# Optimization experiments

Measured on AMD Instinct MI355X. Metric: run time of the kernel, lower is better.

The kernel has to match this reference:

```python
import jax, jax.numpy as jnp
import numpy as np

B, N, F = 8, 500000, 1000000


def setup_inputs() -> dict:
    key = jax.random.key(0)
    k1, k2 = jax.random.split(key)
    vert = jax.random.normal(k1, (B, N, 3), dtype=jnp.float32)
    faces = jax.random.randint(k2, (F, 3), 0, N, dtype=jnp.int64)
    return {"vert": vert, "faces": faces}


def _uniform_laplacian(vert, faces):
    # vert: [B, N, 3], faces: [F, 3]
    n = vert.shape[1]
    i, j, k = faces[:, 0], faces[:, 1], faces[:, 2]
    # 6 directed edges per face: dst accumulates its neighbors' positions (src)
    dst = jnp.concatenate([i, i, j, j, k, k])  # [6F]
    src = jnp.concatenate([j, k, i, k, i, j])  # [6F]
    deg = jax.ops.segment_sum(jnp.ones_like(dst, dtype=vert.dtype), dst, num_segments=n)  # [N]
    nbr_sum = jax.vmap(lambda v: jax.ops.segment_sum(v[src], dst, num_segments=n))(vert)  # [B,N,3]
    # lap = mean(neighbors) - v  (uniform Laplacian: D^{-1} A - I)
    return nbr_sum / jnp.maximum(deg, 1.0)[None, :, None] - vert


def reference(vert, faces):
    lap = _uniform_laplacian(vert, faces)          # [B, N, 3]
    curve = jnp.sqrt(jnp.sum(lap * lap, axis=-1))  # [B, N] (L2 norm over xyz)
    return curve
```

## Files before the change

kernel.cpp:

```cpp
#include <hip/hip_runtime.h>
#include <hip/hip_fp16.h>
#include <math.h>

#define BATCH 8
#define NBUK_MAX 512
#define BSHIFT 10
#define CAPB 6656
#define PACK_MASK 0x7FFFFull
#define SCAN_T 256
#define SCAN_E 8
#define SCAN_TILE (SCAN_T * SCAN_E)

union H2U { __half2 h; unsigned u; };

__device__ __forceinline__ long long pack3(int v, int a, int b) {
    return (long long)(((unsigned long long)(unsigned)v) |
                       ((unsigned long long)(unsigned)a << 19) |
                       ((unsigned long long)(unsigned)b << 38));
}

__global__ __launch_bounds__(1024) void expand_repack_kernel(
        const int* __restrict__ faces,
        int* __restrict__ cursor,
        long long* __restrict__ recbuf,
        const float* __restrict__ vert,
        uint2* __restrict__ vh,
        int N, int F, int expBlocks) {
    if ((int)blockIdx.x < expBlocks) {
        __shared__ int hist[NBUK_MAX];
        __shared__ int sbuf[NBUK_MAX];
        __shared__ int lbase[NBUK_MAX];
        __shared__ int gb[NBUK_MAX];
        __shared__ long long stage[3072];
        int tid = threadIdx.x;
        for (int x = tid; x < NBUK_MAX; x += 1024) hist[x] = 0;
        __syncthreads();

        int f = blockIdx.x * 1024 + tid;
        bool valid = f < F;
        int bb0 = 0, bb1 = 0, bb2 = 0, rr0 = 0, rr1 = 0, rr2 = 0;
        long long rc0 = 0, rc1 = 0, rc2 = 0;
        if (valid) {
            int i = faces[3 * f + 0];
            int j = faces[3 * f + 1];
            int k = faces[3 * f + 2];
            rc0 = pack3(i, j, k);
            rc1 = pack3(j, i, k);
            rc2 = pack3(k, i, j);
            bb0 = i >> BSHIFT; bb1 = j >> BSHIFT; bb2 = k >> BSHIFT;
            rr0 = atomicAdd(&hist[bb0], 1);
            rr1 = atomicAdd(&hist[bb1], 1);
            rr2 = atomicAdd(&hist[bb2], 1);
        }
        __syncthreads();

        if (tid < NBUK_MAX) sbuf[tid] = hist[tid];
        __syncthreads();
        for (int d = 1; d < NBUK_MAX; d <<= 1) {
            int t = 0;
            if (tid < NBUK_MAX && tid >= d) t = sbuf[tid - d];
            __syncthreads();
            if (tid < NBUK_MAX) sbuf[tid] += t;
            __syncthreads();
        }
        if (tid < NBUK_MAX) {
            lbase[tid] = sbuf[tid] - hist[tid];
            gb[tid] = (hist[tid] > 0) ? atomicAdd(&cursor[tid * 16], hist[tid]) : 0;
        }
        __syncthreads();

        if (valid) {
            stage[lbase[bb0] + rr0] = rc0;
            stage[lbase[bb1] + rr1] = rc1;
            stage[lbase[bb2] + rr2] = rc2;
        }
        __syncthreads();

        int total = sbuf[NBUK_MAX - 1];
        for (int t = tid; t < total; t += 1024) {
            long long r = stage[t];
            int v = (int)((unsigned long long)r & PACK_MASK);
            int b = v >> BSHIFT;
            int gpos = gb[b] + (t - lbase[b]);
            if (gpos < CAPB)
                recbuf[(size_t)b * CAPB + gpos] = r;
        }
    } else {
        int u = (blockIdx.x - expBlocks) * 1024 + threadIdx.x;
        if (u < N * BATCH) {
            int v = u >> 3;
            int b = u & 7;
            size_t src = ((size_t)b * N + v) * 3;
            H2U xy, zw;
            xy.h = __floats2half2_rn(vert[src], vert[src + 1]);
            zw.h = __floats2half2_rn(vert[src + 2], 0.0f);
            uint2 w; w.x = xy.u; w.y = zw.u;
            vh[u] = w;
        }
    }
}

__global__ __launch_bounds__(1024) void bucket_build_kernel(
        const int* __restrict__ cursor,
        const long long* __restrict__ recbuf,
        int* __restrict__ cnt, int* __restrict__ off, int* __restrict__ col,
        int N, int NB) {
    __shared__ int cu[NBUK_MAX];
    __shared__ int cntL[1024];
    __shared__ int2 colbuf[CAPB];
    int tid = threadIdx.x;
    int bid = blockIdx.x;

    if (tid < NBUK_MAX) {
        int c = (tid < NB) ? cursor[tid * 16] : 0;
        cu[tid] = c < CAPB ? c : CAPB;
    }
    __syncthreads();
    for (int d = 1; d < NBUK_MAX; d <<= 1) {
        int t = 0;
        if (tid < NBUK_MAX && tid >= d) t = cu[tid - d];
        __syncthreads();
        if (tid < NBUK_MAX) cu[tid] += t;
        __syncthreads();
    }
    int excl = (bid > 0) ? cu[bid - 1] : 0;
    int rcnt = cu[bid] - excl;
    int base_edge = excl * 2;
    int v0 = bid << BSHIFT;
    int nv = N - v0; if (nv > 1024) nv = 1024;

    cntL[tid] = 0;
    __syncthreads();
    const long long* recs = recbuf + (size_t)bid * CAPB;
    for (int x = tid; x < rcnt; x += 1024) {
        int v = (int)((unsigned long long)recs[x] & PACK_MASK);
        atomicAdd(&cntL[v & 1023], 2);
    }
    __syncthreads();

    int myc = cntL[tid];
    if (tid < nv) cnt[v0 + tid] = myc;
    for (int d = 1; d < 1024; d <<= 1) {
        int t = (tid >= d) ? cntL[tid - d] : 0;
        __syncthreads();
        cntL[tid] += t;
        __syncthreads();
    }
    int myoff = cntL[tid] - myc;
    __syncthreads();
    cntL[tid] = myoff;
    if (tid < nv) off[v0 + tid] = base_edge + myoff;
    __syncthreads();

    for (int x = tid; x < rcnt; x += 1024) {
        unsigned long long r = (unsigned long long)recs[x];
        int v = (int)(r & PACK_MASK);
        int a = (int)((r >> 19) & PACK_MASK);
        int b = (int)((r >> 38) & PACK_MASK);
        int p = atomicAdd(&cntL[v & 1023], 2);
        colbuf[p >> 1] = make_int2(a, b);
    }
    __syncthreads();
    int2* c2 = (int2*)col;
    int base2 = base_edge >> 1;
    for (int x = tid; x < rcnt; x += 1024)
        c2[base2 + x] = colbuf[x];
}

__device__ __forceinline__ void unpack_acc(uint2 r, float& ax, float& ay, float& az) {
    H2U xy, zw; xy.u = r.x; zw.u = r.y;
    float2 f0 = __half22float2(xy.h);
    float2 f1 = __half22float2(zw.h);
    ax += f0.x; ay += f0.y; az += f1.x;
}

__global__ void gather_kernel(const uint2* __restrict__ vh,
                              const int* __restrict__ cnt,
                              const int* __restrict__ off,
                              const int* __restrict__ col,
                              float* __restrict__ out, int N) {
    int t = blockIdx.x * blockDim.x + threadIdx.x;
    if (t >= N * BATCH) return;
    int v = t >> 3;
    int b = t & 7;

    int c = cnt[v];
    int start = off[v];
    const int2* c2 = (const int2*)col;
    int e0 = start >> 1;
    int e1 = (start + c) >> 1;

    float ax = 0.f, ay = 0.f, az = 0.f;
    int e = e0;
    for (; e + 4 <= e1; e += 4) {
        int2 s01 = c2[e];
        int2 s23 = c2[e + 1];
        int2 s45 = c2[e + 2];
        int2 s67 = c2[e + 3];
        uint2 r0 = vh[((size_t)s01.x << 3) + b];
        uint2 r1 = vh[((size_t)s01.y << 3) + b];
        uint2 r2 = vh[((size_t)s23.x << 3) + b];
        uint2 r3 = vh[((size_t)s23.y << 3) + b];
        uint2 r4 = vh[((size_t)s45.x << 3) + b];
        uint2 r5 = vh[((size_t)s45.y << 3) + b];
        uint2 r6 = vh[((size_t)s67.x << 3) + b];
        uint2 r7 = vh[((size_t)s67.y << 3) + b];
        unpack_acc(r0, ax, ay, az); unpack_acc(r1, ax, ay, az);
        unpack_acc(r2, ax, ay, az); unpack_acc(r3, ax, ay, az);
        unpack_acc(r4, ax, ay, az); unpack_acc(r5, ax, ay, az);
        unpack_acc(r6, ax, ay, az); unpack_acc(r7, ax, ay, az);
    }
    for (; e < e1; ++e) {
        int2 ss = c2[e];
        uint2 r0 = vh[((size_t)ss.x << 3) + b];
        uint2 r1 = vh[((size_t)ss.y << 3) + b];
        unpack_acc(r0, ax, ay, az);
        unpack_acc(r1, ax, ay, az);
    }

    float invd = 1.0f / fmaxf((float)c, 1.0f);
    float sx = 0.f, sy = 0.f, sz = 0.f;
    unpack_acc(vh[t], sx, sy, sz);
    float l0 = ax * invd - sx;
    float l1 = ay * invd - sy;
    float l2 = az * invd - sz;
    out[(size_t)b * N + v] = sqrtf(l0 * l0 + l1 * l1 + l2 * l2);
}


__global__ void count_only_kernel(const int* __restrict__ faces, int* __restrict__ cnt,
                                  int* __restrict__ rank, int F) {
    int f = blockIdx.x * blockDim.x + threadIdx.x;
    if (f >= F) return;
    rank[3 * f + 0] = atomicAdd(&cnt[faces[3 * f + 0]], 2);
    rank[3 * f + 1] = atomicAdd(&cnt[faces[3 * f + 1]], 2);
    rank[3 * f + 2] = atomicAdd(&cnt[faces[3 * f + 2]], 2);
}

__global__ void scan_sums_kernel(const int* __restrict__ cnt, int* __restrict__ bsums, int N) {
    __shared__ int sh[SCAN_T];
    int base = blockIdx.x * SCAN_TILE + threadIdx.x * SCAN_E;
    int s = 0;
    #pragma unroll
    for (int e = 0; e < SCAN_E; ++e)
        if (base + e < N) s += cnt[base + e];
    sh[threadIdx.x] = s;
    __syncthreads();
    for (int d = SCAN_T / 2; d > 0; d >>= 1) {
        if (threadIdx.x < (unsigned)d) sh[threadIdx.x] += sh[threadIdx.x + d];
        __syncthreads();
    }
    if (threadIdx.x == 0) bsums[blockIdx.x] = sh[0];
}

__global__ void scan_apply_kernel(const int* __restrict__ cnt, int* __restrict__ off,
                                  const int* __restrict__ bsums, int N, int nb) {
    __shared__ int shb[SCAN_T];
    __shared__ int sh[SCAN_T];
    int bv = ((int)threadIdx.x < nb) ? bsums[threadIdx.x] : 0;
    shb[threadIdx.x] = bv;
    __syncthreads();
    for (int d = 1; d < SCAN_T; d <<= 1) {
        int t = (threadIdx.x >= (unsigned)d) ? shb[threadIdx.x - d] : 0;
        __syncthreads();
        shb[threadIdx.x] += t;
        __syncthreads();
    }
    int block_prefix = (blockIdx.x > 0) ? shb[blockIdx.x - 1] : 0;

    int base = blockIdx.x * SCAN_TILE + threadIdx.x * SCAN_E;
    int vals[SCAN_E];
    int s = 0;
    #pragma unroll
    for (int e = 0; e < SCAN_E; ++e) {
        int v = (base + e < N) ? cnt[base + e] : 0;
        vals[e] = v; s += v;
    }
    sh[threadIdx.x] = s;
    __syncthreads();
    for (int d = 1; d < SCAN_T; d <<= 1) {
        int t = (threadIdx.x >= (unsigned)d) ? sh[threadIdx.x - d] : 0;
        __syncthreads();
        sh[threadIdx.x] += t;
        __syncthreads();
    }
    int excl = block_prefix + ((threadIdx.x > 0) ? sh[threadIdx.x - 1] : 0);
    #pragma unroll
    for (int e = 0; e < SCAN_E; ++e) {
        if (base + e < N) off[base + e] = excl;
        excl += vals[e];
    }
}

__global__ void fill_kernel(const int* __restrict__ faces, const int* __restrict__ off,
                            const int* __restrict__ rank, int* __restrict__ col, int F) {
    int f = blockIdx.x * blockDim.x + threadIdx.x;
    if (f >= F) return;
    int i = faces[3 * f + 0];
    int j = faces[3 * f + 1];
    int k = faces[3 * f + 2];
    int2* c2 = (int2*)col;
    c2[(off[i] + rank[3 * f + 0]) >> 1] = make_int2(j, k);
    c2[(off[j] + rank[3 * f + 1]) >> 1] = make_int2(i, k);
    c2[(off[k] + rank[3 * f + 2]) >> 1] = make_int2(i, j);
}

__global__ void gather_scalar_kernel(const float* __restrict__ vert,
                                     const int* __restrict__ cnt,
                                     const int* __restrict__ off,
                                     const int* __restrict__ col,
                                     float* __restrict__ out, int N) {
    int v = blockIdx.x * blockDim.x + threadIdx.x;
    if (v >= N) return;
    int c = cnt[v];
    int start = off[v];
    int end = start + c;
    float ax[BATCH], ay[BATCH], az[BATCH];
    #pragma unroll
    for (int b = 0; b < BATCH; ++b) { ax[b] = 0.f; ay[b] = 0.f; az[b] = 0.f; }
    for (int e = start; e < end; ++e) {
        int s = col[e];
        #pragma unroll
        for (int b = 0; b < BATCH; ++b) {
            size_t base = ((size_t)b * N + s) * 3;
            ax[b] += vert[base + 0];
            ay[b] += vert[base + 1];
            az[b] += vert[base + 2];
        }
    }
    float invd = 1.0f / fmaxf((float)c, 1.0f);
    #pragma unroll
    for (int b = 0; b < BATCH; ++b) {
        size_t base = ((size_t)b * N + v) * 3;
        float l0 = ax[b] * invd - vert[base + 0];
        float l1 = ay[b] * invd - vert[base + 1];
        float l2 = az[b] * invd - vert[base + 2];
        out[(size_t)b * N + v] = sqrtf(l0 * l0 + l1 * l1 + l2 * l2);
    }
}


static inline size_t align256(size_t x) { return (x + 255) & ~(size_t)255; }

extern "C" void kernel_launch(void* const* d_in, const int* in_sizes, int n_in,
                              void* d_out, int out_size, void* d_ws, size_t ws_size,
                              hipStream_t stream) {
    const float* vert  = (const float*)d_in[0];
    const int*   faces = (const int*)d_in[1];
    float*       out   = (float*)d_out;

    int N = out_size / BATCH;
    int F = in_sizes[1] / 3;
    int E = 6 * F;
    int NB = (N + (1 << BSHIFT) - 1) >> BSHIFT;

    char* ws = (char*)d_ws;

    size_t o_cursor = 0;
    size_t o_cnt    = NBUK_MAX * 64;
    size_t o_off    = o_cnt + align256((size_t)N * 4);
    size_t o_col    = o_off + align256((size_t)N * 4);
    size_t o_vh     = o_col + align256((size_t)E * 4);
    size_t o_rec    = o_vh + align256((size_t)N * BATCH * sizeof(uint2));
    size_t need     = o_rec + (size_t)NB * CAPB * 8;

    if (ws_size >= need && N <= 524288 && NB <= NBUK_MAX) {
        int*       cursor = (int*)(ws + o_cursor);
        int*       cnt    = (int*)(ws + o_cnt);
        int*       off    = (int*)(ws + o_off);
        int*       col    = (int*)(ws + o_col);
        uint2*     vh     = (uint2*)(ws + o_vh);
        long long* rec    = (long long*)(ws + o_rec);

        (void)hipMemsetAsync(cursor, 0, NBUK_MAX * 64, stream);

        int expB = (F + 1023) / 1024;
        int repB = (N * BATCH + 1023) / 1024;
        expand_repack_kernel<<<expB + repB, 1024, 0, stream>>>(
            faces, cursor, rec, vert, vh, N, F, expB);

        bucket_build_kernel<<<NB, 1024, 0, stream>>>(cursor, rec, cnt, off, col, N, NB);

        int total = N * BATCH;
        gather_kernel<<<(total + 255) / 256, 256, 0, stream>>>(vh, cnt, off, col, out, N);
        return;
    }

    int threads = 256;
    int nb = (N + SCAN_TILE - 1) / SCAN_TILE;
    size_t f_cnt   = 0;
    size_t f_off   = align256((size_t)N * 4);
    size_t f_bsums = f_off + align256((size_t)N * 4);
    size_t f_col   = f_bsums + 4096;
    size_t f_rank  = f_col + align256((size_t)E * 4);

    int* cnt   = (int*)(ws + f_cnt);
    int* off   = (int*)(ws + f_off);
    int* bsums = (int*)(ws + f_bsums);
    int* col   = (int*)(ws + f_col);
    int* rank  = (int*)(ws + f_rank);

    (void)hipMemsetAsync(cnt, 0, (size_t)N * 4, stream);

    int cntBlocks = (F + threads - 1) / threads;
    count_only_kernel<<<cntBlocks, threads, 0, stream>>>(faces, cnt, rank, F);
    scan_sums_kernel<<<nb, SCAN_T, 0, stream>>>(cnt, bsums, N);
    scan_apply_kernel<<<nb, SCAN_T, 0, stream>>>(cnt, off, bsums, N, nb);
    fill_kernel<<<cntBlocks, threads, 0, stream>>>(faces, off, rank, col, F);
    gather_scalar_kernel<<<(N + threads - 1) / threads, threads, 0, stream>>>(
        vert, cnt, off, col, out, N);
}
```

Before: 246.4 us.

## Fuse bucket CSR build and neighbor gather into one LDS-resident kernel

Merges the bucket build and gather kernels so that each 1024-vertex bucket builds its adjacency in shared memory and then gathers neighbor positions directly from that LDS column buffer. This removes the global writes and reads of cnt/off/col arrays, the cross-bucket prefix scan, and one kernel launch. The trade-off is that gather parallelism drops to only NB (~489) blocks of 1024 threads, each looping 8 times, with large LDS use limiting occupancy, so latency hiding for random vh loads may suffer.

```diff
diff --git a/kernel.cpp b/kernel.cpp
--- a/kernel.cpp
+++ b/kernel.cpp
@@ -100,34 +100,27 @@
     }
 }
 
-__global__ __launch_bounds__(1024) void bucket_build_kernel(
+__device__ __forceinline__ void unpack_acc(uint2 r, float& ax, float& ay, float& az) {
+    H2U xy, zw; xy.u = r.x; zw.u = r.y;
+    float2 f0 = __half22float2(xy.h);
+    float2 f1 = __half22float2(zw.h);
+    ax += f0.x; ay += f0.y; az += f1.x;
+}
+
+__global__ __launch_bounds__(1024) void bucket_gather_kernel(
         const int* __restrict__ cursor,
         const long long* __restrict__ recbuf,
-        int* __restrict__ cnt, int* __restrict__ off, int* __restrict__ col,
-        int N, int NB) {
-    __shared__ int cu[NBUK_MAX];
+        const uint2* __restrict__ vh,
+        float* __restrict__ out, int N) {
     __shared__ int cntL[1024];
+    __shared__ int offL[1024];
     __shared__ int2 colbuf[CAPB];
     int tid = threadIdx.x;
     int bid = blockIdx.x;
-
-    if (tid < NBUK_MAX) {
-        int c = (tid < NB) ? cursor[tid * 16] : 0;
-        cu[tid] = c < CAPB ? c : CAPB;
-    }
-    __syncthreads();
-    for (int d = 1; d < NBUK_MAX; d <<= 1) {
-        int t = 0;
-        if (tid < NBUK_MAX && tid >= d) t = cu[tid - d];
-        __syncthreads();
-        if (tid < NBUK_MAX) cu[tid] += t;
-        __syncthreads();
-    }
-    int excl = (bid > 0) ? cu[bid - 1] : 0;
-    int rcnt = cu[bid] - excl;
-    int base_edge = excl * 2;
     int v0 = bid << BSHIFT;
-    int nv = N - v0; if (nv > 1024) nv = 1024;
+
+    int rc = cursor[bid * 16];
+    int rcnt = rc < CAPB ? rc : CAPB;
 
     cntL[tid] = 0;
     __syncthreads();
@@ -139,7 +132,6 @@
     __syncthreads();
 
     int myc = cntL[tid];
-    if (tid < nv) cnt[v0 + tid] = myc;
     for (int d = 1; d < 1024; d <<= 1) {
         int t = (tid >= d) ? cntL[tid - d] : 0;
         __syncthreads();
@@ -147,9 +139,8 @@
         __syncthreads();
     }
     int myoff = cntL[tid] - myc;
-    __syncthreads();
     cntL[tid] = myoff;
-    if (tid < nv) off[v0 + tid] = base_edge + myoff;
+    offL[tid] = myoff;
     __syncthreads();
 
     for (int x = tid; x < rcnt; x += 1024) {
@@ -161,70 +152,52 @@
         colbuf[p >> 1] = make_int2(a, b);
     }
     __syncthreads();
-    int2* c2 = (int2*)col;
-    int base2 = base_edge >> 1;
-    for (int x = tid; x < rcnt; x += 1024)
-        c2[base2 + x] = colbuf[x];
-}
-
-__device__ __forceinline__ void unpack_acc(uint2 r, float& ax, float& ay, float& az) {
-    H2U xy, zw; xy.u = r.x; zw.u = r.y;
-    float2 f0 = __half22float2(xy.h);
-    float2 f1 = __half22float2(zw.h);
-    ax += f0.x; ay += f0.y; az += f1.x;
-}
-
-__global__ void gather_kernel(const uint2* __restrict__ vh,
-                              const int* __restrict__ cnt,
-                              const int* __restrict__ off,
-                              const int* __restrict__ col,
-                              float* __restrict__ out, int N) {
-    int t = blockIdx.x * blockDim.x + threadIdx.x;
-    if (t >= N * BATCH) return;
-    int v = t >> 3;
-    int b = t & 7;
-
-    int c = cnt[v];
-    int start = off[v];
-    const int2* c2 = (const int2*)col;
-    int e0 = start >> 1;
-    int e1 = (start + c) >> 1;
-
-    float ax = 0.f, ay = 0.f, az = 0.f;
-    int e = e0;
-    for (; e + 4 <= e1; e += 4) {
-        int2 s01 = c2[e];
-        int2 s23 = c2[e + 1];
-        int2 s45 = c2[e + 2];
-        int2 s67 = c2[e + 3];
-        uint2 r0 = vh[((size_t)s01.x << 3) + b];
-        uint2 r1 = vh[((size_t)s01.y << 3) + b];
-        uint2 r2 = vh[((size_t)s23.x << 3) + b];
-        uint2 r3 = vh[((size_t)s23.y << 3) + b];
-        uint2 r4 = vh[((size_t)s45.x << 3) + b];
-        uint2 r5 = vh[((size_t)s45.y << 3) + b];
-        uint2 r6 = vh[((size_t)s67.x << 3) + b];
-        uint2 r7 = vh[((size_t)s67.y << 3) + b];
-        unpack_acc(r0, ax, ay, az); unpack_acc(r1, ax, ay, az);
-        unpack_acc(r2, ax, ay, az); unpack_acc(r3, ax, ay, az);
-        unpack_acc(r4, ax, ay, az); unpack_acc(r5, ax, ay, az);
-        unpack_acc(r6, ax, ay, az); unpack_acc(r7, ax, ay, az);
-    }
-    for (; e < e1; ++e) {
-        int2 ss = c2[e];
-        uint2 r0 = vh[((size_t)ss.x << 3) + b];
-        uint2 r1 = vh[((size_t)ss.y << 3) + b];
-        unpack_acc(r0, ax, ay, az);
-        unpack_acc(r1, ax, ay, az);
-    }
-
-    float invd = 1.0f / fmaxf((float)c, 1.0f);
-    float sx = 0.f, sy = 0.f, sz = 0.f;
-    unpack_acc(vh[t], sx, sy, sz);
-    float l0 = ax * invd - sx;
-    float l1 = ay * invd - sy;
-    float l2 = az * invd - sz;
-    out[(size_t)b * N + v] = sqrtf(l0 * l0 + l1 * l1 + l2 * l2);
+
+    int b = tid & 7;
+    for (int it = 0; it < (1 << BSHIFT) / 128; ++it) {
+        int lv = (tid >> 3) + 128 * it;
+        int v = v0 + lv;
+        if (v >= N) continue;
+        int start = offL[lv];
+        int end = cntL[lv];
+        int c = end - start;
+        int e = start >> 1, e1 = end >> 1;
+
+        float ax = 0.f, ay = 0.f, az = 0.f;
+        for (; e + 4 <= e1; e += 4) {
+            int2 s01 = colbuf[e];
+            int2 s23 = colbuf[e + 1];
+            int2 s45 = colbuf[e + 2];
+            int2 s67 = colbuf[e + 3];
+            uint2 r0 = vh[((size_t)s01.x << 3) + b];
+            uint2 r1 = vh[((size_t)s01.y << 3) + b];
+            uint2 r2 = vh[((size_t)s23.x << 3) + b];
+            uint2 r3 = vh[((size_t)s23.y << 3) + b];
+            uint2 r4 = vh[((size_t)s45.x << 3) + b];
+            uint2 r5 = vh[((size_t)s45.y << 3) + b];
+            uint2 r6 = vh[((size_t)s67.x << 3) + b];
+            uint2 r7 = vh[((size_t)s67.y << 3) + b];
+            unpack_acc(r0, ax, ay, az); unpack_acc(r1, ax, ay, az);
+            unpack_acc(r2, ax, ay, az); unpack_acc(r3, ax, ay, az);
+            unpack_acc(r4, ax, ay, az); unpack_acc(r5, ax, ay, az);
+            unpack_acc(r6, ax, ay, az); unpack_acc(r7, ax, ay, az);
+        }
+        for (; e < e1; ++e) {
+            int2 ss = colbuf[e];
+            uint2 r0 = vh[((size_t)ss.x << 3) + b];
+            uint2 r1 = vh[((size_t)ss.y << 3) + b];
+            unpack_acc(r0, ax, ay, az);
+            unpack_acc(r1, ax, ay, az);
+        }
+
+        float invd = 1.0f / fmaxf((float)c, 1.0f);
+        float sx = 0.f, sy = 0.f, sz = 0.f;
+        unpack_acc(vh[((size_t)v << 3) + b], sx, sy, sz);
+        float l0 = ax * invd - sx;
+        float l1 = ay * invd - sy;
+        float l2 = az * invd - sz;
+        out[(size_t)b * N + v] = sqrtf(l0 * l0 + l1 * l1 + l2 * l2);
+    }
 }
 
 
@@ -357,18 +330,12 @@
     char* ws = (char*)d_ws;
 
     size_t o_cursor = 0;
-    size_t o_cnt    = NBUK_MAX * 64;
-    size_t o_off    = o_cnt + align256((size_t)N * 4);
-    size_t o_col    = o_off + align256((size_t)N * 4);
-    size_t o_vh     = o_col + align256((size_t)E * 4);
+    size_t o_vh     = NBUK_MAX * 64;
     size_t o_rec    = o_vh + align256((size_t)N * BATCH * sizeof(uint2));
     size_t need     = o_rec + (size_t)NB * CAPB * 8;
 
     if (ws_size >= need && N <= 524288 && NB <= NBUK_MAX) {
         int*       cursor = (int*)(ws + o_cursor);
-        int*       cnt    = (int*)(ws + o_cnt);
-        int*       off    = (int*)(ws + o_off);
-        int*       col    = (int*)(ws + o_col);
         uint2*     vh     = (uint2*)(ws + o_vh);
         long long* rec    = (long long*)(ws + o_rec);
 
@@ -379,10 +346,7 @@
         expand_repack_kernel<<<expB + repB, 1024, 0, stream>>>(
             faces, cursor, rec, vert, vh, N, F, expB);
 
-        bucket_build_kernel<<<NB, 1024, 0, stream>>>(cursor, rec, cnt, off, col, N, NB);
-
-        int total = N * BATCH;
-        gather_kernel<<<(total + 255) / 256, 256, 0, stream>>>(vh, cnt, off, col, out, N);
+        bucket_gather_kernel<<<NB, 1024, 0, stream>>>(cursor, rec, vh, out, N);
         return;
     }
 
```

After: 236.0 us. 4.2% less time.
